# Kernel tuning notes

Measured on AMD Instinct MI355X. Metric: run time of the kernel, lower is better.

Reference implementation:

```python
import jax, jax.numpy as jnp
import numpy as np

HID = 4096
NH = 64
HD = HID // NH            # 64
ROT = int(0.5 * HD)       # 32, partial rotary
THETA = 25000.0
EPS = 1e-5
NEG = jnp.finfo(jnp.float32).min


def setup_inputs() -> dict:
    key = jax.random.key(0)
    ks = jax.random.split(key, 8)
    B, S = 1, 2048
    hidden_states = jax.random.normal(ks[0], (B, S, HID), dtype=jnp.float32)
    # causal additive mask [B,1,S,S]
    causal = jnp.where(jnp.tril(jnp.ones((S, S), dtype=bool)), 0.0, NEG)
    attention_mask = jnp.broadcast_to(causal, (B, 1, S, S)).astype(jnp.float32)
    position_ids = jnp.broadcast_to(jnp.arange(S, dtype=jnp.int32), (B, S))
    sc = 1.0 / np.sqrt(HID)
    W_qkv = jax.random.normal(ks[1], (HID, 3 * HID), dtype=jnp.float32) * sc
    b_qkv = jnp.zeros((3 * HID,), dtype=jnp.float32)
    W_dense = jax.random.normal(ks[2], (HID, HID), dtype=jnp.float32) * sc
    b_dense = jnp.zeros((HID,), dtype=jnp.float32)
    q_ln_w = jnp.ones((HD,), dtype=jnp.float32)
    q_ln_b = jnp.zeros((HD,), dtype=jnp.float32)
    k_ln_w = jnp.ones((HD,), dtype=jnp.float32)
    k_ln_b = jnp.zeros((HD,), dtype=jnp.float32)
    return dict(hidden_states=hidden_states, attention_mask=attention_mask,
                position_ids=position_ids, W_qkv=W_qkv, b_qkv=b_qkv,
                W_dense=W_dense, b_dense=b_dense,
                q_ln_w=q_ln_w, q_ln_b=q_ln_b, k_ln_w=k_ln_w, k_ln_b=k_ln_b)


def _layernorm(x, w, b):
    mu = jnp.mean(x, axis=-1, keepdims=True)
    var = jnp.mean(jnp.square(x - mu), axis=-1, keepdims=True)
    return (x - mu) * jax.lax.rsqrt(var + EPS) * w + b


def _rope_cos_sin(seq_len, position_ids):
    inv_freq = 1.0 / (THETA ** (jnp.arange(0, ROT, 2, dtype=jnp.float32) / ROT))
    t = jnp.arange(seq_len, dtype=jnp.float32)
    freqs = jnp.einsum('s,f->sf', t, inv_freq)        # [S, ROT/2]
    emb = jnp.concatenate([freqs, freqs], axis=-1)    # [S, ROT]
    cos = jnp.cos(emb)[position_ids][:, None, :, :]   # [B,1,S,ROT]
    sin = jnp.sin(emb)[position_ids][:, None, :, :]
    return cos, sin


def _rotate_half(x):
    x1, x2 = jnp.split(x, 2, axis=-1)
    return jnp.concatenate([-x2, x1], axis=-1)


def reference(hidden_states, attention_mask, position_ids, W_qkv, b_qkv,
              W_dense, b_dense, q_ln_w, q_ln_b, k_ln_w, k_ln_b):
    B, S, _ = hidden_states.shape
    fused = hidden_states @ W_qkv + b_qkv                 # [B,S,3*HID]
    fused = fused.reshape(B, S, NH, 3, HD)
    q, k, v = fused[..., 0, :], fused[..., 1, :], fused[..., 2, :]  # [B,S,NH,HD]
    q = _layernorm(q, q_ln_w, q_ln_b)
    k = _layernorm(k, k_ln_w, k_ln_b)
    q = q.transpose(0, 2, 1, 3)                           # [B,NH,S,HD]
    k = k.transpose(0, 2, 1, 3)
    v = v.transpose(0, 2, 1, 3)
    cos, sin = _rope_cos_sin(S, position_ids)
    q_rot, q_pass = q[..., :ROT], q[..., ROT:]
    k_rot, k_pass = k[..., :ROT], k[..., ROT:]
    q_rot = q_rot * cos + _rotate_half(q_rot) * sin
    k_rot = k_rot * cos + _rotate_half(k_rot) * sin
    q = jnp.concatenate([q_rot, q_pass], axis=-1)
    k = jnp.concatenate([k_rot, k_pass], axis=-1)
    scores = jnp.einsum('bhqd,bhkd->bhqk', q, k) / np.sqrt(HD)
    scores = scores + attention_mask
    probs = jax.nn.softmax(scores.astype(jnp.float32), axis=-1).astype(q.dtype)
    attn = jnp.einsum('bhqk,bhkd->bhqd', probs, v)        # [B,NH,S,HD]
    attn = attn.transpose(0, 2, 1, 3).reshape(B, S, HID)
    return attn @ W_dense + b_dense
```

## Files before the change

kernel.cpp:

```cpp
#include <hip/hip_runtime.h>
#include <hip/hip_bf16.h>


typedef __attribute__((ext_vector_type(4))) unsigned int u32x4;
typedef __attribute__((ext_vector_type(8))) __bf16 bf16x8;
typedef __attribute__((ext_vector_type(4))) float f32x4;

__device__ __forceinline__ bf16x8 frag_ld(const __hip_bfloat16* p) {
  return __builtin_bit_cast(bf16x8, *(const u32x4*)p);
}

__device__ __forceinline__ void gll16(const __hip_bfloat16* g,
                                      __hip_bfloat16* l) {
  __builtin_amdgcn_global_load_lds(
      (const __attribute__((address_space(1))) unsigned int*)g,
      (__attribute__((address_space(3))) unsigned int*)l, 16, 0, 0);
}

__global__ __launch_bounds__(256) void cvt_kernel(
    const float* __restrict__ in, __hip_bfloat16* __restrict__ out, int n4) {
  int i = blockIdx.x * 256 + threadIdx.x;
  if (i < n4) {
    float4 v = ((const float4*)in)[i];
    union { __hip_bfloat16 h[4]; unsigned long long u; } pk;
    pk.h[0] = __float2bfloat16(v.x);
    pk.h[1] = __float2bfloat16(v.y);
    pk.h[2] = __float2bfloat16(v.z);
    pk.h[3] = __float2bfloat16(v.w);
    ((unsigned long long*)out)[i] = pk.u;
  }
}

__global__ __launch_bounds__(256) void transpose_kernel(
    const float* __restrict__ W, __hip_bfloat16* __restrict__ WT,
    int K, int ldW, int colStride, int colOff) {
  __shared__ __align__(16) __hip_bfloat16 tile[64 * 72];
  const int t = threadIdx.x;
  const int c0 = blockIdx.x * colStride + colOff;
  const int n0 = blockIdx.x * 64;
  const int k0 = blockIdx.y * 64;
  for (int c = t; c < 1024; c += 256) {
    int row = c >> 4, col4 = (c & 15) << 2;
    float4 v = *(const float4*)&W[(size_t)(k0 + row) * ldW + c0 + col4];
    union { __hip_bfloat16 h[4]; unsigned long long u; } pk;
    pk.h[0] = __float2bfloat16(v.x);
    pk.h[1] = __float2bfloat16(v.y);
    pk.h[2] = __float2bfloat16(v.z);
    pk.h[3] = __float2bfloat16(v.w);
    *(unsigned long long*)&tile[row * 72 + col4] = pk.u;
  }
  __syncthreads();
  for (int c = t; c < 512; c += 256) {
    int row = c >> 3, col8 = (c & 7) << 3;
    union { __hip_bfloat16 h[8]; u32x4 v; } pk;
#pragma unroll
    for (int j = 0; j < 8; ++j) pk.h[j] = tile[(col8 + j) * 72 + row];
    *(u32x4*)&WT[(size_t)(n0 + row) * K + k0 + col8] = pk.v;
  }
}

__global__ __launch_bounds__(256) void gemm_bt_kernel(
    const __hip_bfloat16* __restrict__ A, const __hip_bfloat16* __restrict__ BT,
    const float* __restrict__ bias, float* __restrict__ Cf,
    __hip_bfloat16* __restrict__ Cb, int M, int N, int K, int mode) {
  __shared__ __align__(16) __hip_bfloat16 Als[128 * 32];
  __shared__ __align__(16) __hip_bfloat16 Bls[128 * 32];
  const int t = threadIdx.x;
  const int m0 = blockIdx.y * 128, n0 = blockIdx.x * 128;
  const int wv = t >> 6, lane = t & 63;
  const int qd = lane >> 4, md = lane & 15;
  const int wm = (wv >> 1) * 64, wn = (wv & 1) * 64;
  f32x4 acc[4][4] = {};
  const int row0 = t >> 2, col0 = (t & 3) << 3;
  const __hip_bfloat16* gA0 = A + (size_t)(m0 + row0) * K + col0;
  const __hip_bfloat16* gA1 = gA0 + (size_t)64 * K;
  const __hip_bfloat16* gB0 = BT + (size_t)(n0 + row0) * K + col0;
  const __hip_bfloat16* gB1 = gB0 + (size_t)64 * K;
  __hip_bfloat16* lA0 = Als + wv * 512;
  __hip_bfloat16* lA1 = Als + 2048 + wv * 512;
  __hip_bfloat16* lB0 = Bls + wv * 512;
  __hip_bfloat16* lB1 = Bls + 2048 + wv * 512;
  for (int k0 = 0; k0 < K; k0 += 32) {
    __syncthreads();
    gll16(gA0 + k0, lA0);
    gll16(gA1 + k0, lA1);
    gll16(gB0 + k0, lB0);
    gll16(gB1 + k0, lB1);
    __syncthreads();
    bf16x8 af[4], bf[4];
#pragma unroll
    for (int i = 0; i < 4; ++i)
      af[i] = frag_ld(&Als[(wm + i * 16 + md) * 32 + qd * 8]);
#pragma unroll
    for (int i = 0; i < 4; ++i)
      bf[i] = frag_ld(&Bls[(wn + i * 16 + md) * 32 + qd * 8]);
#pragma unroll
    for (int mi = 0; mi < 4; ++mi)
#pragma unroll
      for (int ni = 0; ni < 4; ++ni)
        acc[mi][ni] = __builtin_amdgcn_mfma_f32_16x16x32_bf16(
            af[mi], bf[ni], acc[mi][ni], 0, 0, 0);
  }
#pragma unroll
  for (int ni = 0; ni < 4; ++ni) {
    int col = n0 + wn + ni * 16 + md;
    float bv = (mode == 0) ? bias[col] : bias[(col >> 6) * 192 + (col & 63)];
#pragma unroll
    for (int mi = 0; mi < 4; ++mi) {
      int rb = m0 + wm + mi * 16 + qd * 4;
#pragma unroll
      for (int r = 0; r < 4; ++r) {
        float v = acc[mi][ni][r] + bv;
        if (mode == 0)
          Cf[(size_t)(rb + r) * N + col] = v;
        else
          Cb[((size_t)(col >> 6) * M + rb + r) * 64 + (col & 63)] =
              __float2bfloat16(v);
      }
    }
  }
}

__device__ __forceinline__ float wred_sum(float v) {
#pragma unroll
  for (int x = 1; x < 64; x <<= 1) v += __shfl_xor(v, x, 64);
  return v;
}

__global__ __launch_bounds__(256) void lnrope_kernel(
    __hip_bfloat16* __restrict__ Q, __hip_bfloat16* __restrict__ K,
    const __hip_bfloat16* __restrict__ V, __hip_bfloat16* __restrict__ VT,
    const int* __restrict__ pos_ids,
    const float* __restrict__ qw, const float* __restrict__ qb,
    const float* __restrict__ kw, const float* __restrict__ kbias) {
  const int h = blockIdx.x;
  const int s0 = blockIdx.y * 64;
  const int t = threadIdx.x, wv = t >> 6, lane = t & 63;
  const float gq = qw[lane], bqv = qb[lane];
  const float gk = kw[lane], bkv = kbias[lane];
  const float invf = powf(25000.0f, -(float)(lane & 15) / 16.0f);
  for (int i = 0; i < 16; ++i) {
    int s = s0 + wv * 16 + i;
    size_t idx = ((size_t)h * 2048 + s) * 64 + lane;
    float q = (float)Q[idx];
    float k = (float)K[idx];
    float muq = wred_sum(q) * (1.0f / 64.0f);
    float dq = q - muq;
    float vq = wred_sum(dq * dq) * (1.0f / 64.0f);
    float qn = dq * rsqrtf(vq + 1e-5f) * gq + bqv;
    float muk = wred_sum(k) * (1.0f / 64.0f);
    float dk = k - muk;
    float vk = wred_sum(dk * dk) * (1.0f / 64.0f);
    float kn = dk * rsqrtf(vk + 1e-5f) * gk + bkv;
    float ang = (float)pos_ids[s] * invf;
    float sn, cs;
    sincosf(ang, &sn, &cs);
    float qo = __shfl_xor(qn, 16, 64);
    float ko = __shfl_xor(kn, 16, 64);
    float qr = qn, kr = kn;
    if (lane < 16) {
      qr = qn * cs - qo * sn; kr = kn * cs - ko * sn;
    } else if (lane < 32) {
      qr = qn * cs + qo * sn; kr = kn * cs + ko * sn;
    }
    Q[idx] = __float2bfloat16(qr * 0.18033688f);
    K[idx] = __float2bfloat16(kr);
  }
  __shared__ __align__(16) __hip_bfloat16 vt[64 * 72];
  for (int c = t; c < 512; c += 256) {
    int r = c >> 3, col8 = (c & 7) << 3;
    *(u32x4*)&vt[r * 72 + col8] =
        *(const u32x4*)&V[((size_t)h * 2048 + s0 + r) * 64 + col8];
  }
  __syncthreads();
  for (int c = t; c < 512; c += 256) {
    int d = c >> 3, col8 = (c & 7) << 3;
    union { __hip_bfloat16 hh[8]; u32x4 v; } pk;
#pragma unroll
    for (int j = 0; j < 8; ++j) pk.hh[j] = vt[(col8 + j) * 72 + d];
    *(u32x4*)&VT[((size_t)h * 64 + d) * 2048 + s0 + col8] = pk.v;
  }
}

__global__ __launch_bounds__(256) void fattn_kernel(
    const __hip_bfloat16* __restrict__ Q, const __hip_bfloat16* __restrict__ K,
    const __hip_bfloat16* __restrict__ VT, __hip_bfloat16* __restrict__ attn) {
  const int h = blockIdx.x, qb = 31 - blockIdx.y;
  const int t = threadIdx.x, wv = t >> 6, lane = t & 63;
  const int qd = lane >> 4, md = lane & 15;
  __shared__ __align__(16) __hip_bfloat16 Kls[64 * 72];
  __shared__ __align__(16) __hip_bfloat16 Vls[64 * 72];
  __shared__ __align__(16) __hip_bfloat16 Pls[64 * 72];
  const int q0 = qb * 64;
  const __hip_bfloat16* Qp = Q + ((size_t)h * 2048 + q0 + wv * 16 + md) * 64;
  bf16x8 qf0 = frag_ld(Qp + qd * 8);
  bf16x8 qf1 = frag_ld(Qp + 32 + qd * 8);
  float lp[4] = {0.f, 0.f, 0.f, 0.f};
  f32x4 O[4] = {};
  for (int kb = 0; kb <= qb; ++kb) {
    __syncthreads();
    for (int c = t; c < 512; c += 256) {
      int row = c >> 3, col8 = (c & 7) << 3;
      *(u32x4*)&Kls[row * 72 + col8] =
          *(const u32x4*)&K[((size_t)h * 2048 + kb * 64 + row) * 64 + col8];
      *(u32x4*)&Vls[row * 72 + col8] =
          *(const u32x4*)&VT[((size_t)h * 64 + row) * 2048 + kb * 64 + col8];
    }
    __syncthreads();
    const bool diag = (kb == qb);
    float pv[4][4];
#pragma unroll
    for (int nt = 0; nt < 4; ++nt) {
      f32x4 s4 = {};
      bf16x8 kf0 = frag_ld(&Kls[(nt * 16 + md) * 72 + qd * 8]);
      bf16x8 kf1 = frag_ld(&Kls[(nt * 16 + md) * 72 + 32 + qd * 8]);
      s4 = __builtin_amdgcn_mfma_f32_16x16x32_bf16(qf0, kf0, s4, 0, 0, 0);
      s4 = __builtin_amdgcn_mfma_f32_16x16x32_bf16(qf1, kf1, s4, 0, 0, 0);
      int key = nt * 16 + md;
#pragma unroll
      for (int r = 0; r < 4; ++r) {
        float p = exp2f(s4[r]);
        if (diag) p = (key > wv * 16 + qd * 4 + r) ? 0.f : p;
        pv[nt][r] = p;
        lp[r] += p;
      }
    }
#pragma unroll
    for (int nt = 0; nt < 4; ++nt)
#pragma unroll
      for (int r = 0; r < 4; ++r)
        Pls[(wv * 16 + qd * 4 + r) * 72 + nt * 16 + md] =
            __float2bfloat16(pv[nt][r]);
    bf16x8 pf0 = frag_ld(&Pls[(wv * 16 + md) * 72 + qd * 8]);
    bf16x8 pf1 = frag_ld(&Pls[(wv * 16 + md) * 72 + 32 + qd * 8]);
#pragma unroll
    for (int nt = 0; nt < 4; ++nt) {
      bf16x8 vf0 = frag_ld(&Vls[(nt * 16 + md) * 72 + qd * 8]);
      bf16x8 vf1 = frag_ld(&Vls[(nt * 16 + md) * 72 + 32 + qd * 8]);
      O[nt] = __builtin_amdgcn_mfma_f32_16x16x32_bf16(pf0, vf0, O[nt], 0, 0, 0);
      O[nt] = __builtin_amdgcn_mfma_f32_16x16x32_bf16(pf1, vf1, O[nt], 0, 0, 0);
    }
  }
#pragma unroll
  for (int r = 0; r < 4; ++r) {
#pragma unroll
    for (int x = 1; x < 16; x <<= 1) lp[r] += __shfl_xor(lp[r], x, 16);
    lp[r] = 1.0f / lp[r];
  }
#pragma unroll
  for (int nt = 0; nt < 4; ++nt) {
    int col = h * 64 + nt * 16 + md;
#pragma unroll
    for (int r = 0; r < 4; ++r) {
      int row = q0 + wv * 16 + qd * 4 + r;
      attn[(size_t)row * 4096 + col] = __float2bfloat16(O[nt][r] * lp[r]);
    }
  }
}

extern "C" void kernel_launch(void* const* d_in, const int* in_sizes, int n_in,
                              void* d_out, int out_size, void* d_ws,
                              size_t ws_size, hipStream_t stream) {
  const float* hidden = (const float*)d_in[0];
  const int* pos = (const int*)d_in[2];
  const float* Wqkv = (const float*)d_in[3];
  const float* bqkv = (const float*)d_in[4];
  const float* Wd = (const float*)d_in[5];
  const float* bd = (const float*)d_in[6];
  const float* qlw = (const float*)d_in[7];
  const float* qlb = (const float*)d_in[8];
  const float* klw = (const float*)d_in[9];
  const float* klb = (const float*)d_in[10];

  char* ws = (char*)d_ws;
  __hip_bfloat16* WpT = (__hip_bfloat16*)ws;
  __hip_bfloat16* VT = (__hip_bfloat16*)ws;
  __hip_bfloat16* attn = (__hip_bfloat16*)(ws + 16777216);
  __hip_bfloat16* Hb = (__hip_bfloat16*)(ws + 33554432);
  __hip_bfloat16* Qb = (__hip_bfloat16*)(ws + 50331648);
  __hip_bfloat16* Kb = (__hip_bfloat16*)(ws + 67108864);
  __hip_bfloat16* Vb = (__hip_bfloat16*)(ws + 83886080);
  __hip_bfloat16* WdT = (__hip_bfloat16*)(ws + 33554432);
  float* out = (float*)d_out;

  cvt_kernel<<<8192, 256, 0, stream>>>(hidden, Hb, 2097152);
  __hip_bfloat16* qkv_dst[3] = {Qb, Kb, Vb};
  for (int p = 0; p < 3; ++p) {
    transpose_kernel<<<dim3(64, 64), 256, 0, stream>>>(Wqkv, WpT, 4096, 12288,
                                                       192, p * 64);
    gemm_bt_kernel<<<dim3(32, 16), 256, 0, stream>>>(
        Hb, WpT, bqkv + p * 64, nullptr, qkv_dst[p], 2048, 4096, 4096, 1);
  }
  lnrope_kernel<<<dim3(64, 32), 256, 0, stream>>>(Qb, Kb, Vb, VT, pos, qlw, qlb,
                                                  klw, klb);
  fattn_kernel<<<dim3(64, 32), 256, 0, stream>>>(Qb, Kb, VT, attn);
  transpose_kernel<<<dim3(64, 64), 256, 0, stream>>>(Wd, WdT, 4096, 4096, 64, 0);
  gemm_bt_kernel<<<dim3(32, 16), 256, 0, stream>>>(attn, WdT, bd, out, nullptr,
                                                   2048, 4096, 4096, 0);
}
```

Baseline: 911.3 us.

## Replace GEMM with 128x256 triple-buffered pipelined kernel using swizzled LDS

Replaces the simple 128x128, K=32 single-buffered GEMM with a 512-thread 128x256 tile kernel using K=64 steps, a three-stage LDS ring buffer with prefetch two stages ahead, XOR-swizzled LDS layout to avoid bank conflicts, interleaved global loads between MFMA phases, setprio hints, and a block-index swizzle for L2 locality. It targets exposed memory latency and barrier stalls in the QKV and output projections. Risks include heavy LDS use (about 144KB per block) that limits occupancy, and the hardcoded 64 K-steps and grid shape that only work for K=4096 and 2048x4096.

```diff
diff --git a/kernel.cpp b/kernel.cpp
--- a/kernel.cpp
+++ b/kernel.cpp
@@ -59,55 +59,110 @@
   }
 }
 
-__global__ __launch_bounds__(256) void gemm_bt_kernel(
+__global__ __launch_bounds__(512, 2) void gemm256_kernel(
     const __hip_bfloat16* __restrict__ A, const __hip_bfloat16* __restrict__ BT,
     const float* __restrict__ bias, float* __restrict__ Cf,
     __hip_bfloat16* __restrict__ Cb, int M, int N, int K, int mode) {
-  __shared__ __align__(16) __hip_bfloat16 Als[128 * 32];
-  __shared__ __align__(16) __hip_bfloat16 Bls[128 * 32];
+  __shared__ __align__(16) __hip_bfloat16 As[3][128 * 64];
+  __shared__ __align__(16) __hip_bfloat16 Bs[3][256 * 64];
   const int t = threadIdx.x;
-  const int m0 = blockIdx.y * 128, n0 = blockIdx.x * 128;
   const int wv = t >> 6, lane = t & 63;
   const int qd = lane >> 4, md = lane & 15;
-  const int wm = (wv >> 1) * 64, wn = (wv & 1) * 64;
+  const int wr = wv >> 2, wc = wv & 3;
+  const int bid = blockIdx.x;
+  const int swz = (bid & 7) * 32 + (bid >> 3);
+  const int m0 = (swz >> 4) * 128, n0 = (swz & 15) * 256;
+  const int rA = t >> 3;
+  const int cg = (t & 7) ^ (rA & 7);
+  const __hip_bfloat16* pA0 = A + (size_t)(m0 + rA) * K + cg * 8;
+  const __hip_bfloat16* pA1 = A + (size_t)(m0 + 64 + rA) * K + cg * 8;
+  const __hip_bfloat16* pB0 = BT + (size_t)(n0 + rA) * K + cg * 8;
+  const __hip_bfloat16* pB1 = BT + (size_t)(n0 + 64 + rA) * K + cg * 8;
+  const __hip_bfloat16* pB2 = BT + (size_t)(n0 + 128 + rA) * K + cg * 8;
+  const __hip_bfloat16* pB3 = BT + (size_t)(n0 + 192 + rA) * K + cg * 8;
+  const int ldsW = wv * 8 * 64;
+  const int aRow = (wr * 64 + md) * 64;
+  const int bRow = (wc * 64 + md) * 64;
+  const int sw0 = (qd ^ (md & 7)) << 3;
+  const int sw1 = ((4 + qd) ^ (md & 7)) << 3;
   f32x4 acc[4][4] = {};
-  const int row0 = t >> 2, col0 = (t & 3) << 3;
-  const __hip_bfloat16* gA0 = A + (size_t)(m0 + row0) * K + col0;
-  const __hip_bfloat16* gA1 = gA0 + (size_t)64 * K;
-  const __hip_bfloat16* gB0 = BT + (size_t)(n0 + row0) * K + col0;
-  const __hip_bfloat16* gB1 = gB0 + (size_t)64 * K;
-  __hip_bfloat16* lA0 = Als + wv * 512;
-  __hip_bfloat16* lA1 = Als + 2048 + wv * 512;
-  __hip_bfloat16* lB0 = Bls + wv * 512;
-  __hip_bfloat16* lB1 = Bls + 2048 + wv * 512;
-  for (int k0 = 0; k0 < K; k0 += 32) {
-    __syncthreads();
-    gll16(gA0 + k0, lA0);
-    gll16(gA1 + k0, lA1);
-    gll16(gB0 + k0, lB0);
-    gll16(gB1 + k0, lB1);
-    __syncthreads();
+
+  gll16(pA0, &As[0][ldsW]);
+  gll16(pA1, &As[0][64 * 64 + ldsW]);
+  gll16(pB0, &Bs[0][ldsW]);
+  gll16(pB1, &Bs[0][64 * 64 + ldsW]);
+  gll16(pB2, &Bs[0][128 * 64 + ldsW]);
+  gll16(pB3, &Bs[0][192 * 64 + ldsW]);
+  gll16(pA0 + 64, &As[1][ldsW]);
+  gll16(pA1 + 64, &As[1][64 * 64 + ldsW]);
+  gll16(pB0 + 64, &Bs[1][ldsW]);
+  gll16(pB1 + 64, &Bs[1][64 * 64 + ldsW]);
+  gll16(pB2 + 64, &Bs[1][128 * 64 + ldsW]);
+  gll16(pB3 + 64, &Bs[1][192 * 64 + ldsW]);
+  asm volatile("s_waitcnt vmcnt(6)" ::: "memory");
+  __builtin_amdgcn_s_barrier();
+
+  int cur = 0, nb = 2;
+  for (int kt = 0; kt < 64; ++kt) {
+    const __hip_bfloat16* Ac = As[cur];
+    const __hip_bfloat16* Bc = Bs[cur];
+    const bool st = kt < 62;
+    const int koff = (kt + 2) * 64;
     bf16x8 af[4], bf[4];
 #pragma unroll
-    for (int i = 0; i < 4; ++i)
-      af[i] = frag_ld(&Als[(wm + i * 16 + md) * 32 + qd * 8]);
-#pragma unroll
-    for (int i = 0; i < 4; ++i)
-      bf[i] = frag_ld(&Bls[(wn + i * 16 + md) * 32 + qd * 8]);
+    for (int i = 0; i < 4; ++i) af[i] = frag_ld(&Ac[aRow + i * 1024 + sw0]);
+#pragma unroll
+    for (int i = 0; i < 4; ++i) bf[i] = frag_ld(&Bc[bRow + i * 1024 + sw0]);
+    if (st) {
+      gll16(pA0 + koff, &As[nb][ldsW]);
+      gll16(pA1 + koff, &As[nb][64 * 64 + ldsW]);
+      gll16(pB0 + koff, &Bs[nb][ldsW]);
+    }
+    __builtin_amdgcn_s_barrier();
+    asm volatile("s_waitcnt lgkmcnt(0)" ::: "memory");
+    __builtin_amdgcn_s_setprio(1);
 #pragma unroll
     for (int mi = 0; mi < 4; ++mi)
 #pragma unroll
       for (int ni = 0; ni < 4; ++ni)
         acc[mi][ni] = __builtin_amdgcn_mfma_f32_16x16x32_bf16(
             af[mi], bf[ni], acc[mi][ni], 0, 0, 0);
+    __builtin_amdgcn_s_setprio(0);
+    __builtin_amdgcn_s_barrier();
+#pragma unroll
+    for (int i = 0; i < 4; ++i) af[i] = frag_ld(&Ac[aRow + i * 1024 + sw1]);
+#pragma unroll
+    for (int i = 0; i < 4; ++i) bf[i] = frag_ld(&Bc[bRow + i * 1024 + sw1]);
+    if (st) {
+      gll16(pB1 + koff, &Bs[nb][64 * 64 + ldsW]);
+      gll16(pB2 + koff, &Bs[nb][128 * 64 + ldsW]);
+      gll16(pB3 + koff, &Bs[nb][192 * 64 + ldsW]);
+    }
+    __builtin_amdgcn_s_barrier();
+    asm volatile("s_waitcnt lgkmcnt(0)" ::: "memory");
+    __builtin_amdgcn_s_setprio(1);
+#pragma unroll
+    for (int mi = 0; mi < 4; ++mi)
+#pragma unroll
+      for (int ni = 0; ni < 4; ++ni)
+        acc[mi][ni] = __builtin_amdgcn_mfma_f32_16x16x32_bf16(
+            af[mi], bf[ni], acc[mi][ni], 0, 0, 0);
+    __builtin_amdgcn_s_setprio(0);
+    if (kt < 62)
+      asm volatile("s_waitcnt vmcnt(6)" ::: "memory");
+    else if (kt < 63)
+      asm volatile("s_waitcnt vmcnt(0)" ::: "memory");
+    __builtin_amdgcn_s_barrier();
+    cur = (cur == 2) ? 0 : cur + 1;
+    nb = (nb == 2) ? 0 : nb + 1;
   }
 #pragma unroll
   for (int ni = 0; ni < 4; ++ni) {
-    int col = n0 + wn + ni * 16 + md;
+    int col = n0 + wc * 64 + ni * 16 + md;
     float bv = (mode == 0) ? bias[col] : bias[(col >> 6) * 192 + (col & 63)];
 #pragma unroll
     for (int mi = 0; mi < 4; ++mi) {
-      int rb = m0 + wm + mi * 16 + qd * 4;
+      int rb = m0 + wr * 64 + mi * 16 + qd * 4;
 #pragma unroll
       for (int r = 0; r < 4; ++r) {
         float v = acc[mi][ni][r] + bv;
@@ -288,13 +343,13 @@
   for (int p = 0; p < 3; ++p) {
     transpose_kernel<<<dim3(64, 64), 256, 0, stream>>>(Wqkv, WpT, 4096, 12288,
                                                        192, p * 64);
-    gemm_bt_kernel<<<dim3(32, 16), 256, 0, stream>>>(
-        Hb, WpT, bqkv + p * 64, nullptr, qkv_dst[p], 2048, 4096, 4096, 1);
+    gemm256_kernel<<<256, 512, 0, stream>>>(Hb, WpT, bqkv + p * 64, nullptr,
+                                            qkv_dst[p], 2048, 4096, 4096, 1);
   }
   lnrope_kernel<<<dim3(64, 32), 256, 0, stream>>>(Qb, Kb, Vb, VT, pos, qlw, qlb,
                                                   klw, klb);
   fattn_kernel<<<dim3(64, 32), 256, 0, stream>>>(Qb, Kb, VT, attn);
   transpose_kernel<<<dim3(64, 64), 256, 0, stream>>>(Wd, WdT, 4096, 4096, 64, 0);
-  gemm_bt_kernel<<<dim3(32, 16), 256, 0, stream>>>(attn, WdT, bd, out, nullptr,
-                                                   2048, 4096, 4096, 0);
-}
+  gemm256_kernel<<<256, 512, 0, stream>>>(attn, WdT, bd, out, nullptr,
+                                          2048, 4096, 4096, 0);
+}
```

After: 785.3 us. 1.16x faster.
